# Kernel tuning notes

Measured on AMD Instinct MI355X. Metric: run time of the kernel, lower is better.

Reference implementation:

```python
import jax, jax.numpy as jnp
import numpy as np

P = 8.0  # Lp exponent of the distance neuron (finite-p stage of l_inf-dist training)


def _patches(t, k, stride, pad):
    # [B, Cin, H, W] -> [B, Cin*k*k, H', W'], feature dim ordered channel-major
    return jax.lax.conv_general_dilated_patches(
        t, (k, k), (stride, stride), [(pad, pad), (pad, pad)])


def _lp(d):
    # d: [B, Cout, Cin*k*k, H', W'] nonnegative -> Lp norm over patch dim
    return jnp.power(jnp.sum(jnp.power(d, P), axis=2), 1.0 / P)


def norm_dist_conv(x, l, u, w, stride, pad):
    # Lp-distance "convolution": y[b,o,i,j] = || patch(x)[b,:,i,j] - w[o,:] ||_p
    # mean_normalize=True: zero-center each output unit's weight vector
    Cout, Cin, k, _ = w.shape
    wf = w.reshape(Cout, -1)
    wf = wf - jnp.mean(wf, axis=1, keepdims=True)
    wb = wf[None, :, :, None, None]                      # [1, Cout, Ckk, 1, 1]
    px = _patches(x, k, stride, pad)[:, None]            # [B, 1, Ckk, H', W']
    pl = _patches(l, k, stride, pad)[:, None]
    pu = _patches(u, k, stride, pad)[:, None]
    y = _lp(jnp.abs(px - wb))
    # interval bounds of |x_j - w_j| given x_j in [l_j, u_j], then monotone Lp
    dl = jnp.maximum(jnp.maximum(pl - wb, wb - pu), 0.0)
    du = jnp.maximum(jnp.abs(pl - wb), jnp.abs(pu - wb))
    return y, _lp(dl), _lp(du)


def bound_relu(x, l, u):
    # ReLU is monotone: apply elementwise to value and both bounds
    return jax.nn.relu(x), jax.nn.relu(l), jax.nn.relu(u)


def setup_inputs() -> dict:
    key = jax.random.key(0)
    k1, k2, k3 = jax.random.split(key, 3)
    B, C, H, W = 4, 32, 32, 32
    eps = 0.1  # l_inf perturbation radius
    x = jax.random.normal(k1, (B, C, H, W), dtype=jnp.float32)
    lower = x - eps
    upper = x + eps
    scale = 1.0 / np.sqrt(C * 9)
    weight1 = jax.random.normal(k2, (C, C, 3, 3), dtype=jnp.float32) * scale
    weight2 = jax.random.normal(k3, (C, C, 3, 3), dtype=jnp.float32) * scale
    return {"x": x, "lower": lower, "upper": upper,
            "weight1": weight1, "weight2": weight2}


def reference(x, lower, upper, weight1, weight2):
    # conv1 (stride=1, pad=1) -> BoundReLU -> conv2 -> residual add -> BoundReLU
    o = norm_dist_conv(x, lower, upper, weight1, 1, 1)
    o = bound_relu(*o)
    o = norm_dist_conv(*o, weight2, 1, 1)
    out = (o[0] + x, o[1] + lower, o[2] + upper)  # identity shortcut (stride=1, in==out)
    out = bound_relu(*out)
    return jnp.stack(out)  # [3, B, C, H, W]: (value, lower, upper)
```

## Files before the change

### kernel.cpp

```cpp
#include <hip/hip_runtime.h>

#define NB 4
#define NC 32
#define NH 32
#define NW 32
#define KK 288
#define PLANE (NB*NC*NH*NW)
#define CHALF 16

__device__ __forceinline__ float s3(float v) { return sqrtf(sqrtf(sqrtf(v))); }

__global__ __launch_bounds__(256) void prep_weights_k(
        const float* __restrict__ w1, const float* __restrict__ w2,
        float* __restrict__ wf1, float* __restrict__ wf2)
{
    const int row = blockIdx.x;
    const float* src = (row < NC) ? w1 : w2;
    float* dst = (row < NC) ? wf1 : wf2;
    const int co = row & (NC - 1);
    const int tid = threadIdx.x;
    __shared__ float red[256];
    const float a = src[co*KK + tid];
    const float b = (tid + 256 < KK) ? src[co*KK + tid + 256] : 0.0f;
    red[tid] = a + b;
    __syncthreads();
    for (int s = 128; s > 0; s >>= 1) {
        if (tid < s) red[tid] += red[tid + s];
        __syncthreads();
    }
    const float mean = red[0] * (1.0f / (float)KK);
    {
        const int e = tid, c = e / 9, r9 = e - c*9, r = r9 / 3, kw = r9 - r*3;
        dst[co*384 + ((c*3 + r) << 2) + kw] = a - mean;
    }
    if (tid + 256 < KK) {
        const int e = tid + 256, c = e / 9, r9 = e - c*9, r = r9 / 3, kw = r9 - r*3;
        dst[co*384 + ((c*3 + r) << 2) + kw] = b - mean;
    }
}

template<bool STAGE2>
__global__ __launch_bounds__(256, 4) void normdist_conv_k(
    const float* __restrict__ sy,
    const float* __restrict__ sl,
    const float* __restrict__ su,
    const float* __restrict__ wf,
    float* __restrict__ pY, float* __restrict__ pL, float* __restrict__ pU)
{
    const int h     = blockIdx.x;
    const int cog   = blockIdx.y >> 1;
    const int chalf = blockIdx.y & 1;
    const int ch0   = chalf * CHALF;
    const int b     = blockIdx.z;
    const int tx    = threadIdx.x;
    const int ty    = threadIdx.y;
    const int tid   = ty * 32 + tx;

    __shared__ float4 sP[CHALF*3*34];

    for (int i = tid; i < CHALF*3*34; i += 256) {
        const int c   = i / 102;
        const int rem = i - c*102;
        const int r   = rem / 34;
        const int col = rem - r*34;
        const int gh  = h + r - 1;
        const int gw  = col - 1;
        float vx = 0.0f, vl = 0.0f, vu = 0.0f;
        if ((unsigned)gh < NH && (unsigned)gw < NW) {
            const int g = ((b*NC + ch0 + c)*NH + gh)*NW + gw;
            if (STAGE2) {
                vx = s3(sy[g] + sy[PLANE + g]);
                vl = s3(sl[g] + sl[PLANE + g]);
                vu = s3(su[g] + su[PLANE + g]);
            } else {
                vx = sy[g]; vl = sl[g]; vu = su[g];
            }
        }
        sP[i] = make_float4(vx, vl, vu, 0.0f);
    }
    __syncthreads();

    const int co = cog*8 + ty;
    const float4* wbase = (const float4*)wf + (co*NC + ch0)*3;

    float accY = 0.0f, accL = 0.0f, accU = 0.0f;

    auto tap = [&](float wv, float4 p) {
        const float d  = p.x - wv;
        const float d2 = d*d, d4 = d2*d2;
        accY = fmaf(d4, d4, accY);
        const float a  = p.y - wv;
        const float nb = wv - p.z;
        const float m  = fmaxf(fmaxf(a, nb), 0.0f);
        const float m2 = m*m, m4 = m2*m2;
        accL = fmaf(m4, m4, accL);
        const float a2 = a*a, q2 = nb*nb;
        const float mm2 = fmaxf(a2, q2);
        const float mm4 = mm2*mm2;
        accU = fmaf(mm4, mm4, accU);
    };

    #pragma unroll 2
    for (int c = 0; c < CHALF; ++c) {
        const float4 w0 = wbase[c*3 + 0];
        const float4 w1 = wbase[c*3 + 1];
        const float4 w2 = wbase[c*3 + 2];
        const int pb = c*102 + tx;
        tap(w0.x, sP[pb +  0]); tap(w0.y, sP[pb +  1]); tap(w0.z, sP[pb +  2]);
        tap(w1.x, sP[pb + 34]); tap(w1.y, sP[pb + 35]); tap(w1.z, sP[pb + 36]);
        tap(w2.x, sP[pb + 68]); tap(w2.y, sP[pb + 69]); tap(w2.z, sP[pb + 70]);
    }

    const int o = ((b*NC + co)*NH + h)*NW + tx;
    pY[chalf*PLANE + o] = accY;
    pL[chalf*PLANE + o] = accL;
    pU[chalf*PLANE + o] = accU;
}

__global__ __launch_bounds__(256) void epilogue_k(
    const float* __restrict__ pY, const float* __restrict__ pL, const float* __restrict__ pU,
    const float* __restrict__ x,  const float* __restrict__ l,  const float* __restrict__ u,
    float* __restrict__ out)
{
    const int o = blockIdx.x*256 + threadIdx.x;
    const float y  = s3(pY[o] + pY[PLANE + o]);
    const float dl = s3(pL[o] + pL[PLANE + o]);
    const float du = s3(pU[o] + pU[PLANE + o]);
    out[o]           = fmaxf(y  + x[o], 0.0f);
    out[PLANE + o]   = fmaxf(dl + l[o], 0.0f);
    out[2*PLANE + o] = fmaxf(du + u[o], 0.0f);
}

extern "C" void kernel_launch(void* const* d_in, const int* in_sizes, int n_in,
                              void* d_out, int out_size, void* d_ws, size_t ws_size,
                              hipStream_t stream)
{
    const float* x  = (const float*)d_in[0];
    const float* l  = (const float*)d_in[1];
    const float* u  = (const float*)d_in[2];
    const float* w1 = (const float*)d_in[3];
    const float* w2 = (const float*)d_in[4];
    float* ws  = (float*)d_ws;
    float* wf1 = ws;
    float* wf2 = wf1 + 12288;
    float* p1Y = wf2 + 12288;
    float* p1L = p1Y + 2*PLANE;
    float* p1U = p1L + 2*PLANE;
    float* p2Y = p1U + 2*PLANE;
    float* p2L = p2Y + 2*PLANE;
    float* p2U = p2L + 2*PLANE;
    float* out = (float*)d_out;

    prep_weights_k<<<64, 256, 0, stream>>>(w1, w2, wf1, wf2);

    dim3 blk(32, 8);
    dim3 grd(NH, 8, NB);
    normdist_conv_k<false><<<grd, blk, 0, stream>>>(x, l, u, wf1, p1Y, p1L, p1U);
    normdist_conv_k<true ><<<grd, blk, 0, stream>>>(p1Y, p1L, p1U, wf2, p2Y, p2L, p2U);
    epilogue_k<<<PLANE/256, 256, 0, stream>>>(p2Y, p2L, p2U, x, l, u, out);
}
```

Baseline: 107.3 us.

## Compute two output channels per thread and vectorize epilogue with float4

Each conv thread now accumulates two output channels (co and co+8), so each shared-memory patch read is used twice and the grid's channel-group dimension is halved. Weights for the next input channel are prefetched into registers, and launch bounds drop to 2 blocks/SM to allow the larger register footprint. The epilogue processes four elements per thread with float4 loads and stores. The trade-off is fewer blocks and lower occupancy on a GPU with many CUs.

```diff
diff --git a/kernel.cpp b/kernel.cpp
--- a/kernel.cpp
+++ b/kernel.cpp
@@ -40,7 +40,7 @@
 }
 
 template<bool STAGE2>
-__global__ __launch_bounds__(256, 4) void normdist_conv_k(
+__global__ __launch_bounds__(256, 2) void normdist_conv_k(
     const float* __restrict__ sy,
     const float* __restrict__ sl,
     const float* __restrict__ su,
@@ -80,12 +80,15 @@
     }
     __syncthreads();
 
-    const int co = cog*8 + ty;
-    const float4* wbase = (const float4*)wf + (co*NC + ch0)*3;
-
-    float accY = 0.0f, accL = 0.0f, accU = 0.0f;
-
-    auto tap = [&](float wv, float4 p) {
+    const int co0 = cog*16 + ty;
+    const int co1 = co0 + 8;
+    const float4* wbA = (const float4*)wf + (co0*NC + ch0)*3;
+    const float4* wbB = (const float4*)wf + (co1*NC + ch0)*3;
+
+    float aY0 = 0.0f, aL0 = 0.0f, aU0 = 0.0f;
+    float aY1 = 0.0f, aL1 = 0.0f, aU1 = 0.0f;
+
+    auto tap = [&](float wv, float4 p, float& accY, float& accL, float& accU) {
         const float d  = p.x - wv;
         const float d2 = d*d, d4 = d2*d2;
         accY = fmaf(d4, d4, accY);
@@ -100,21 +103,38 @@
         accU = fmaf(mm4, mm4, accU);
     };
 
-    #pragma unroll 2
+    float4 cA0 = wbA[0], cA1 = wbA[1], cA2 = wbA[2];
+    float4 cB0 = wbB[0], cB1 = wbB[1], cB2 = wbB[2];
+
     for (int c = 0; c < CHALF; ++c) {
-        const float4 w0 = wbase[c*3 + 0];
-        const float4 w1 = wbase[c*3 + 1];
-        const float4 w2 = wbase[c*3 + 2];
+        const int cn = (c < CHALF-1) ? c + 1 : c;
+        const float4 nA0 = wbA[cn*3+0], nA1 = wbA[cn*3+1], nA2 = wbA[cn*3+2];
+        const float4 nB0 = wbB[cn*3+0], nB1 = wbB[cn*3+1], nB2 = wbB[cn*3+2];
+
         const int pb = c*102 + tx;
-        tap(w0.x, sP[pb +  0]); tap(w0.y, sP[pb +  1]); tap(w0.z, sP[pb +  2]);
-        tap(w1.x, sP[pb + 34]); tap(w1.y, sP[pb + 35]); tap(w1.z, sP[pb + 36]);
-        tap(w2.x, sP[pb + 68]); tap(w2.y, sP[pb + 69]); tap(w2.z, sP[pb + 70]);
-    }
-
-    const int o = ((b*NC + co)*NH + h)*NW + tx;
-    pY[chalf*PLANE + o] = accY;
-    pL[chalf*PLANE + o] = accL;
-    pU[chalf*PLANE + o] = accU;
+        const float4 p00 = sP[pb +  0], p01 = sP[pb +  1], p02 = sP[pb +  2];
+        const float4 p10 = sP[pb + 34], p11 = sP[pb + 35], p12 = sP[pb + 36];
+        const float4 p20 = sP[pb + 68], p21 = sP[pb + 69], p22 = sP[pb + 70];
+
+        tap(cA0.x, p00, aY0, aL0, aU0); tap(cA0.y, p01, aY0, aL0, aU0); tap(cA0.z, p02, aY0, aL0, aU0);
+        tap(cB0.x, p00, aY1, aL1, aU1); tap(cB0.y, p01, aY1, aL1, aU1); tap(cB0.z, p02, aY1, aL1, aU1);
+        tap(cA1.x, p10, aY0, aL0, aU0); tap(cA1.y, p11, aY0, aL0, aU0); tap(cA1.z, p12, aY0, aL0, aU0);
+        tap(cB1.x, p10, aY1, aL1, aU1); tap(cB1.y, p11, aY1, aL1, aU1); tap(cB1.z, p12, aY1, aL1, aU1);
+        tap(cA2.x, p20, aY0, aL0, aU0); tap(cA2.y, p21, aY0, aL0, aU0); tap(cA2.z, p22, aY0, aL0, aU0);
+        tap(cB2.x, p20, aY1, aL1, aU1); tap(cB2.y, p21, aY1, aL1, aU1); tap(cB2.z, p22, aY1, aL1, aU1);
+
+        cA0 = nA0; cA1 = nA1; cA2 = nA2;
+        cB0 = nB0; cB1 = nB1; cB2 = nB2;
+    }
+
+    const int o0 = ((b*NC + co0)*NH + h)*NW + tx;
+    const int o1 = o0 + 8*NH*NW;
+    pY[chalf*PLANE + o0] = aY0;
+    pL[chalf*PLANE + o0] = aL0;
+    pU[chalf*PLANE + o0] = aU0;
+    pY[chalf*PLANE + o1] = aY1;
+    pL[chalf*PLANE + o1] = aL1;
+    pU[chalf*PLANE + o1] = aU1;
 }
 
 __global__ __launch_bounds__(256) void epilogue_k(
@@ -122,13 +142,38 @@
     const float* __restrict__ x,  const float* __restrict__ l,  const float* __restrict__ u,
     float* __restrict__ out)
 {
-    const int o = blockIdx.x*256 + threadIdx.x;
-    const float y  = s3(pY[o] + pY[PLANE + o]);
-    const float dl = s3(pL[o] + pL[PLANE + o]);
-    const float du = s3(pU[o] + pU[PLANE + o]);
-    out[o]           = fmaxf(y  + x[o], 0.0f);
-    out[PLANE + o]   = fmaxf(dl + l[o], 0.0f);
-    out[2*PLANE + o] = fmaxf(du + u[o], 0.0f);
+    const int i = blockIdx.x*256 + threadIdx.x;
+    const float4* pY4 = (const float4*)pY;
+    const float4* pL4 = (const float4*)pL;
+    const float4* pU4 = (const float4*)pU;
+    const float4* x4  = (const float4*)x;
+    const float4* l4  = (const float4*)l;
+    const float4* u4  = (const float4*)u;
+    float4* out4 = (float4*)out;
+    const int Q = PLANE/4;
+
+    const float4 ya = pY4[i], yb = pY4[Q + i];
+    const float4 la = pL4[i], lb = pL4[Q + i];
+    const float4 ua = pU4[i], ub = pU4[Q + i];
+    const float4 xr = x4[i], lr = l4[i], ur = u4[i];
+
+    float4 oy, ol, ou;
+    oy.x = fmaxf(s3(ya.x + yb.x) + xr.x, 0.0f);
+    oy.y = fmaxf(s3(ya.y + yb.y) + xr.y, 0.0f);
+    oy.z = fmaxf(s3(ya.z + yb.z) + xr.z, 0.0f);
+    oy.w = fmaxf(s3(ya.w + yb.w) + xr.w, 0.0f);
+    ol.x = fmaxf(s3(la.x + lb.x) + lr.x, 0.0f);
+    ol.y = fmaxf(s3(la.y + lb.y) + lr.y, 0.0f);
+    ol.z = fmaxf(s3(la.z + lb.z) + lr.z, 0.0f);
+    ol.w = fmaxf(s3(la.w + lb.w) + lr.w, 0.0f);
+    ou.x = fmaxf(s3(ua.x + ub.x) + ur.x, 0.0f);
+    ou.y = fmaxf(s3(ua.y + ub.y) + ur.y, 0.0f);
+    ou.z = fmaxf(s3(ua.z + ub.z) + ur.z, 0.0f);
+    ou.w = fmaxf(s3(ua.w + ub.w) + ur.w, 0.0f);
+
+    out4[i]       = oy;
+    out4[Q + i]   = ol;
+    out4[2*Q + i] = ou;
 }
 
 extern "C" void kernel_launch(void* const* d_in, const int* in_sizes, int n_in,
@@ -154,8 +199,8 @@
     prep_weights_k<<<64, 256, 0, stream>>>(w1, w2, wf1, wf2);
 
     dim3 blk(32, 8);
-    dim3 grd(NH, 8, NB);
+    dim3 grd(NH, 4, NB);
     normdist_conv_k<false><<<grd, blk, 0, stream>>>(x, l, u, wf1, p1Y, p1L, p1U);
     normdist_conv_k<true ><<<grd, blk, 0, stream>>>(p1Y, p1L, p1U, wf2, p2Y, p2L, p2U);
-    epilogue_k<<<PLANE/256, 256, 0, stream>>>(p2Y, p2L, p2U, x, l, u, out);
-}
+    epilogue_k<<<PLANE/1024, 256, 0, stream>>>(p2Y, p2L, p2U, x, l, u, out);
+}
```

After: 108.0 us. About the same (+0.7%).
